# Optimization experiments

Hardware: AMD Instinct MI355X
Metric: run time of the kernel (lower is better)

## Reference

```python
import jax, jax.numpy as jnp
import numpy as np

N = 50000
E = 800000
NFEAT, NHID, NCODE, NCLASS = 512, 256, 64, 40


def setup_inputs() -> dict:
    key = jax.random.key(0)
    ks = jax.random.split(key, 16)
    def glorot(k, shape):
        lim = 1.0 / np.sqrt(shape[0])
        return jax.random.uniform(k, shape, jnp.float32, -lim, lim)
    return {
        "x": jax.random.normal(ks[0], (N, NFEAT), jnp.float32),
        "edge_src": jax.random.randint(ks[1], (E,), 0, N, jnp.int32),
        "edge_dst": jax.random.randint(ks[2], (E,), 0, N, jnp.int32),
        "edge_weight": jax.random.uniform(ks[3], (E,), jnp.float32),
        "eps": jax.random.normal(ks[4], (N, NCODE), jnp.float32),
        # gc1: GraphConvolution(nfeat, nhid)
        "W1": glorot(ks[5], (NFEAT, NHID)),
        "b1": glorot(ks[6], (NHID,)),
        # fc11 / fc12: Linear(nhid, ncode)
        "W_mu": glorot(ks[7], (NHID, NCODE)),
        "b_mu": glorot(ks[8], (NCODE,)),
        "W_lv": glorot(ks[9], (NHID, NCODE)),
        "b_lv": glorot(ks[10], (NCODE,)),
        # fc2: Linear(ncode, nhid)
        "W_dec": glorot(ks[11], (NCODE, NHID)),
        "b_dec": glorot(ks[12], (NHID,)),
        # gc2: GraphConvolution(2*nhid, nclass)
        "W2": glorot(ks[13], (2 * NHID, NCLASS)),
        "b2": glorot(ks[14], (NCLASS,)),
    }


def spmm(edge_src, edge_dst, edge_weight, support):
    # spmm(adj, support): gather rows at src, scale by edge weight, scatter-add to dst
    msgs = support[edge_src] * edge_weight[:, None]  # [E, d]
    return jax.ops.segment_sum(msgs, edge_dst, num_segments=N)


def reference(x, edge_src, edge_dst, edge_weight, eps,
              W1, b1, W_mu, b_mu, W_lv, b_lv, W_dec, b_dec, W2, b2):
    # gc1: relu(spmm(adj, x @ W1) + b1)
    h1 = jax.nn.relu(spmm(edge_src, edge_dst, edge_weight, x @ W1) + b1)
    # dropout is identity in inference mode
    mu = h1 @ W_mu + b_mu
    log_var = h1 @ W_lv + b_lv
    # reparametrize: std = exp(log_var) (as in source, no 0.5 factor)
    z = mu + eps * jnp.exp(log_var)
    # decode
    x1 = jax.nn.relu(z @ W_dec + b_dec)
    x1 = jnp.concatenate([x1, h1], axis=1)  # [N, 2*nhid]
    # gc2
    logits = spmm(edge_src, edge_dst, edge_weight, x1 @ W2) + b2
    return jax.nn.log_softmax(logits, axis=1)
```

## Files before the change

kernel.cpp:

```cpp
#include <hip/hip_runtime.h>
#include <math.h>

#define N_NODES 50000
#define N_EDGES 800000
#define NFEAT 512
#define NHID 256
#define NCODE 64
#define NCLASS 40
#define NCLS_PAD 48
#define NB_SCAN 196

typedef __attribute__((ext_vector_type(8))) short short8;
typedef __attribute__((ext_vector_type(8))) unsigned short ushort8;
typedef __attribute__((ext_vector_type(4))) unsigned short ushort4v;
typedef __attribute__((ext_vector_type(4))) float floatx4;

__device__ inline unsigned short f2bf(float f) {
    unsigned u = __builtin_bit_cast(unsigned, f);
    u += 0x7fff + ((u >> 16) & 1);
    return (unsigned short)(u >> 16);
}
__device__ inline float bf2f(unsigned short h) {
    return __builtin_bit_cast(float, (unsigned)h << 16);
}
__device__ inline unsigned pkbf(float lo, float hi) {
    unsigned r;
    asm("v_cvt_pk_bf16_f32 %0, %1, %2" : "=v"(r) : "v"(lo), "v"(hi));
    return r;
}
__device__ inline void gload_lds16(const void* g, void* l) {
    __builtin_amdgcn_global_load_lds(
        (const __attribute__((address_space(1))) unsigned int*)g,
        (__attribute__((address_space(3))) unsigned int*)l, 16, 0, 0);
}

__global__ __launch_bounds__(256) void hist_kernel(const int* __restrict__ dst,
                                                   int* __restrict__ counts) {
    int t = blockIdx.x * 256 + threadIdx.x;
    if (t < N_EDGES) atomicAdd(&counts[dst[t]], 1);
}

__global__ __launch_bounds__(256) void scan_block_sums(const int* __restrict__ counts,
                                                       int* __restrict__ blockSums) {
    __shared__ int red[256];
    int t = threadIdx.x;
    int i = blockIdx.x * 256 + t;
    red[t] = (i < N_NODES) ? counts[i] : 0;
    __syncthreads();
#pragma unroll
    for (int off = 128; off > 0; off >>= 1) {
        if (t < off) red[t] += red[t + off];
        __syncthreads();
    }
    if (t == 0) blockSums[blockIdx.x] = red[0];
}

__global__ __launch_bounds__(256) void scan_block_offsets(const int* __restrict__ blockSums,
                                                          int* __restrict__ blockOffsets,
                                                          int* __restrict__ offsets) {
    __shared__ int s[256];
    int t = threadIdx.x;
    int v = (t < NB_SCAN) ? blockSums[t] : 0;
    s[t] = v;
    __syncthreads();
#pragma unroll
    for (int off = 1; off < 256; off <<= 1) {
        int x = (t >= off) ? s[t - off] : 0;
        __syncthreads();
        s[t] += x;
        __syncthreads();
    }
    if (t < NB_SCAN) blockOffsets[t] = s[t] - v;
    if (t == 255) offsets[N_NODES] = s[255];
}

__global__ __launch_bounds__(256) void scan_final(const int* __restrict__ counts,
                                                  const int* __restrict__ blockOffsets,
                                                  int* __restrict__ offsets) {
    __shared__ int s[256];
    int t = threadIdx.x;
    int i = blockIdx.x * 256 + t;
    int v = (i < N_NODES) ? counts[i] : 0;
    s[t] = v;
    __syncthreads();
#pragma unroll
    for (int off = 1; off < 256; off <<= 1) {
        int x = (t >= off) ? s[t - off] : 0;
        __syncthreads();
        s[t] += x;
        __syncthreads();
    }
    if (i < N_NODES) offsets[i] = blockOffsets[blockIdx.x] + s[t] - v;
}

__global__ __launch_bounds__(256) void scatter_kernel(const int* __restrict__ dst,
                                                      const int* __restrict__ src,
                                                      const float* __restrict__ w,
                                                      const int* __restrict__ offsets,
                                                      int* __restrict__ cursor,
                                                      int2* __restrict__ edges) {
    int t = blockIdx.x * 256 + threadIdx.x;
    if (t < N_EDGES) {
        int d = dst[t];
        int pos = offsets[d] + atomicAdd(&cursor[d], 1);
        edges[pos] = make_int2(src[t], __builtin_bit_cast(int, w[t]));
    }
}

__global__ __launch_bounds__(256) void wprep_kernel(const float* __restrict__ W1,
                                                    const float* __restrict__ W2,
                                                    const float* __restrict__ W_mu,
                                                    const float* __restrict__ W_lv,
                                                    const float* __restrict__ W_dec,
                                                    unsigned short* __restrict__ W1t,
                                                    unsigned short* __restrict__ W2bt,
                                                    unsigned short* __restrict__ W_mulvt,
                                                    unsigned short* __restrict__ W_dect) {
    int idx = blockIdx.x * 256 + threadIdx.x;
    if (idx < NFEAT * NHID) {
        int k = idx >> 8;
        int n = idx & 255;
        W1t[(size_t)n * NFEAT + k] = f2bf(W1[idx]);
    } else if (idx < NFEAT * NHID + NCLS_PAD * NFEAT) {
        int i2 = idx - NFEAT * NHID;
        int n = i2 >> 9;
        int k = i2 & 511;
        W2bt[i2] = (n < NCLASS) ? f2bf(W2[(size_t)k * NCLASS + n]) : (unsigned short)0;
    } else if (idx < NFEAT * NHID + NCLS_PAD * NFEAT + 128 * 256) {
        int i2 = idx - NFEAT * NHID - NCLS_PAD * NFEAT;
        int j = i2 >> 8;
        int k = i2 & 255;
        float v = (j < 64) ? W_mu[(size_t)k * NCODE + j] : W_lv[(size_t)k * NCODE + (j - 64)];
        W_mulvt[i2] = f2bf(v);
    } else if (idx < NFEAT * NHID + NCLS_PAD * NFEAT + 128 * 256 + 256 * 64) {
        int i2 = idx - NFEAT * NHID - NCLS_PAD * NFEAT - 128 * 256;
        int n = i2 >> 6;
        int k = i2 & 63;
        W_dect[i2] = f2bf(W_dec[(size_t)k * NHID + n]);
    }
}

__global__ __launch_bounds__(256) void gemm1_mfma(const float* __restrict__ A,
                                                  const unsigned short* __restrict__ Bt,
                                                  unsigned short* __restrict__ C) {
    __shared__ unsigned short As[2][128 * 64];
    __shared__ unsigned short Bs[2][128 * 64];
    int t = threadIdx.x;
    int wave = t >> 6, lane = t & 63;
    int quad = lane >> 4, m16 = lane & 15;
    int wr = wave >> 1, wc = wave & 1;
    int m0 = blockIdx.x * 128;
    int n0 = blockIdx.y * 128;

    int srow = t >> 3;
    int kcs = (t & 7) ^ (srow & 7);
    const float* Ap[4];
    const unsigned short* Bp[4];
#pragma unroll
    for (int r = 0; r < 4; ++r) {
        int row = r * 32 + srow;
        int ga = m0 + row;
        if (ga >= N_NODES) ga = N_NODES - 1;
        Ap[r] = A + (size_t)ga * NFEAT + kcs * 8;
        Bp[r] = Bt + (size_t)(n0 + row) * NFEAT + kcs * 8;
    }

    floatx4 acc[4][4];
#pragma unroll
    for (int m = 0; m < 4; ++m)
#pragma unroll
        for (int n = 0; n < 4; ++n) acc[m][n] = (floatx4){0.f, 0.f, 0.f, 0.f};

    float4 a0[4], a1[4];
#pragma unroll
    for (int r = 0; r < 4; ++r)
        gload_lds16(Bp[r], &Bs[0][(r * 256 + wave * 64) * 8]);
#pragma unroll
    for (int r = 0; r < 4; ++r) {
        a0[r] = *(const float4*)(Ap[r]);
        a1[r] = *(const float4*)(Ap[r] + 4);
    }
#pragma unroll
    for (int r = 0; r < 4; ++r) {
        uint4 w;
        w.x = pkbf(a0[r].x, a0[r].y);
        w.y = pkbf(a0[r].z, a0[r].w);
        w.z = pkbf(a1[r].x, a1[r].y);
        w.w = pkbf(a1[r].z, a1[r].w);
        *(uint4*)&As[0][(r * 256 + t) * 8] = w;
    }
    __syncthreads();

#pragma unroll
    for (int k0 = 0; k0 < NFEAT; k0 += 64) {
        const int cur = (k0 >> 6) & 1, nxt = cur ^ 1;
        const bool more = (k0 + 64 < NFEAT);
        if (more) {
#pragma unroll
            for (int r = 0; r < 4; ++r)
                gload_lds16(Bp[r] + (k0 + 64), &Bs[nxt][(r * 256 + wave * 64) * 8]);
#pragma unroll
            for (int r = 0; r < 4; ++r) {
                a0[r] = *(const float4*)(Ap[r] + k0 + 64);
                a1[r] = *(const float4*)(Ap[r] + k0 + 68);
            }
        }
#pragma unroll
        for (int c = 0; c < 2; ++c) {
            int sw = ((c * 4 + quad) ^ (m16 & 7)) * 8;
            short8 af[4], bfr[4];
#pragma unroll
            for (int m = 0; m < 4; ++m)
                af[m] = *(const short8*)&As[cur][(wr * 64 + m * 16 + m16) * 64 + sw];
#pragma unroll
            for (int n = 0; n < 4; ++n)
                bfr[n] = *(const short8*)&Bs[cur][(wc * 64 + n * 16 + m16) * 64 + sw];
#pragma unroll
            for (int m = 0; m < 4; ++m)
#pragma unroll
                for (int n = 0; n < 4; ++n)
                    acc[m][n] =
                        __builtin_amdgcn_mfma_f32_16x16x32_bf16(af[m], bfr[n], acc[m][n], 0, 0, 0);
        }
        if (more) {
#pragma unroll
            for (int r = 0; r < 4; ++r) {
                uint4 w;
                w.x = pkbf(a0[r].x, a0[r].y);
                w.y = pkbf(a0[r].z, a0[r].w);
                w.z = pkbf(a1[r].x, a1[r].y);
                w.w = pkbf(a1[r].z, a1[r].w);
                *(uint4*)&As[nxt][(r * 256 + t) * 8] = w;
            }
            __syncthreads();
        }
    }
#pragma unroll
    for (int m = 0; m < 4; ++m) {
#pragma unroll
        for (int n = 0; n < 4; ++n) {
            int col = n0 + wc * 64 + n * 16 + m16;
#pragma unroll
            for (int r = 0; r < 4; ++r) {
                int row = m0 + wr * 64 + m * 16 + quad * 4 + r;
                if (row < N_NODES) C[(size_t)row * NHID + col] = f2bf(acc[m][n][r]);
            }
        }
    }
}

__global__ __launch_bounds__(256) void spmm1_kernel(const int* __restrict__ offsets,
                                                    const int2* __restrict__ edges,
                                                    const unsigned short* __restrict__ S1b,
                                                    const float* __restrict__ b1,
                                                    unsigned short* __restrict__ x1cat) {
    int n = blockIdx.x * 4 + (threadIdx.x >> 6);
    int lane = threadIdx.x & 63;
    int beg = offsets[n], end = offsets[n + 1];
    float ax = 0.f, ay = 0.f, az = 0.f, aw = 0.f;
    int i = beg;
    for (; i + 8 <= end; i += 8) {
        int2 e[8];
        ushort4v r[8];
#pragma unroll
        for (int u = 0; u < 8; u++) e[u] = edges[i + u];
#pragma unroll
        for (int u = 0; u < 8; u++)
            r[u] = *(const ushort4v*)&S1b[(size_t)e[u].x * NHID + lane * 4];
#pragma unroll
        for (int u = 0; u < 8; u++) {
            float ww = __builtin_bit_cast(float, e[u].y);
            ax += ww * bf2f(r[u][0]);
            ay += ww * bf2f(r[u][1]);
            az += ww * bf2f(r[u][2]);
            aw += ww * bf2f(r[u][3]);
        }
    }
    for (; i < end; i++) {
        int2 e = edges[i];
        float ww = __builtin_bit_cast(float, e.y);
        ushort4v r = *(const ushort4v*)&S1b[(size_t)e.x * NHID + lane * 4];
        ax += ww * bf2f(r[0]); ay += ww * bf2f(r[1]);
        az += ww * bf2f(r[2]); aw += ww * bf2f(r[3]);
    }
    float4 bb = *(const float4*)&b1[lane * 4];
    ushort4v hb;
    hb[0] = f2bf(fmaxf(ax + bb.x, 0.f));
    hb[1] = f2bf(fmaxf(ay + bb.y, 0.f));
    hb[2] = f2bf(fmaxf(az + bb.z, 0.f));
    hb[3] = f2bf(fmaxf(aw + bb.w, 0.f));
    *(ushort4v*)&x1cat[(size_t)n * (2 * NHID) + NHID + lane * 4] = hb;
}

__global__ __launch_bounds__(256) void mlp_mfma(const unsigned short* __restrict__ x1cat_ro,
                                                const float* __restrict__ eps,
                                                const float* __restrict__ b_mu,
                                                const float* __restrict__ b_lv,
                                                const unsigned short* __restrict__ W_mulvt,
                                                const float* __restrict__ b_dec,
                                                const unsigned short* __restrict__ W_dect,
                                                unsigned short* __restrict__ x1cat) {
    __shared__ float smulv[16][132];
    __shared__ unsigned short z_bf[16][72];
    int t = threadIdx.x;
    int wave = t >> 6, lane = t & 63;
    int quad = lane >> 4, m16 = lane & 15;
    int node0 = blockIdx.x * 16;

    {
        floatx4 acc[2];
        acc[0] = (floatx4){0.f, 0.f, 0.f, 0.f};
        acc[1] = (floatx4){0.f, 0.f, 0.f, 0.f};
        const unsigned short* Abase =
            x1cat_ro + (size_t)(node0 + m16) * 512 + 256 + quad * 8;
        const unsigned short* Bb0 = W_mulvt + (size_t)(wave * 32 + m16) * 256 + quad * 8;
        const unsigned short* Bb1 = Bb0 + 16 * 256;
#pragma unroll
        for (int k0 = 0; k0 < 256; k0 += 32) {
            short8 afrag = *(const short8*)(Abase + k0);
            short8 bf0 = *(const short8*)(Bb0 + k0);
            short8 bf1 = *(const short8*)(Bb1 + k0);
            acc[0] = __builtin_amdgcn_mfma_f32_16x16x32_bf16(afrag, bf0, acc[0], 0, 0, 0);
            acc[1] = __builtin_amdgcn_mfma_f32_16x16x32_bf16(afrag, bf1, acc[1], 0, 0, 0);
        }
#pragma unroll
        for (int nt = 0; nt < 2; nt++) {
            int j = wave * 32 + nt * 16 + m16;
            float bias = (j < 64) ? b_mu[j] : b_lv[j - 64];
#pragma unroll
            for (int r = 0; r < 4; r++)
                smulv[quad * 4 + r][j] = acc[nt][r] + bias;
        }
    }
    __syncthreads();
#pragma unroll
    for (int r = 0; r < 4; r++) {
        int idx = t + r * 256;
        int n = idx >> 6, j = idx & 63;
        float z = smulv[n][j] + eps[(size_t)node0 * NCODE + idx] * expf(smulv[n][64 + j]);
        z_bf[n][j] = f2bf(z);
    }
    __syncthreads();
    {
        floatx4 acc[4];
#pragma unroll
        for (int i = 0; i < 4; i++) acc[i] = (floatx4){0.f, 0.f, 0.f, 0.f};
#pragma unroll
        for (int ks = 0; ks < 2; ks++) {
            int k0 = ks * 32;
            short8 afrag = *(const short8*)&z_bf[m16][k0 + quad * 8];
#pragma unroll
            for (int nt = 0; nt < 4; nt++) {
                int col = wave * 64 + nt * 16 + m16;
                short8 bfrag = *(const short8*)(W_dect + (size_t)col * 64 + k0 + quad * 8);
                acc[nt] = __builtin_amdgcn_mfma_f32_16x16x32_bf16(afrag, bfrag, acc[nt], 0, 0, 0);
            }
        }
#pragma unroll
        for (int nt = 0; nt < 4; nt++) {
            int col = wave * 64 + nt * 16 + m16;
            float bias = b_dec[col];
#pragma unroll
            for (int r = 0; r < 4; r++) {
                int node = node0 + quad * 4 + r;
                x1cat[(size_t)node * 512 + col] = f2bf(fmaxf(acc[nt][r] + bias, 0.f));
            }
        }
    }
}

__global__ __launch_bounds__(256) void gemm2_mfma(const unsigned short* __restrict__ Xb,
                                                  const unsigned short* __restrict__ Bt,
                                                  unsigned short* __restrict__ S2b) {
    __shared__ unsigned short Bs[NCLS_PAD][520];
    int t = threadIdx.x;
    int wave = t >> 6, lane = t & 63;
    int quad = lane >> 4, m16 = lane & 15;
    int m0 = blockIdx.x * 64;

#pragma unroll
    for (int r = 0; r < 12; ++r) {
        int cidx = r * 256 + t;
        int row = cidx >> 6, col = (cidx & 63) * 8;
        *(ushort8*)&Bs[row][col] = *(const ushort8*)&Bt[(size_t)row * NFEAT + col];
    }

    int arow = m0 + wave * 16 + m16;
    if (arow >= N_NODES) arow = N_NODES - 1;
    const unsigned short* Abase = Xb + (size_t)arow * NFEAT + quad * 8;

    floatx4 acc[3];
#pragma unroll
    for (int i = 0; i < 3; i++) acc[i] = (floatx4){0.f, 0.f, 0.f, 0.f};
    __syncthreads();

#pragma unroll
    for (int k0 = 0; k0 < NFEAT; k0 += 32) {
        short8 af = *(const short8*)(Abase + k0);
#pragma unroll
        for (int nt = 0; nt < 3; nt++) {
            short8 bfr = *(const short8*)&Bs[nt * 16 + m16][k0 + quad * 8];
            acc[nt] = __builtin_amdgcn_mfma_f32_16x16x32_bf16(af, bfr, acc[nt], 0, 0, 0);
        }
    }
#pragma unroll
    for (int nt = 0; nt < 3; nt++) {
        int col = nt * 16 + m16;
        if (col < NCLASS) {
#pragma unroll
            for (int r = 0; r < 4; r++) {
                int row = m0 + wave * 16 + quad * 4 + r;
                if (row < N_NODES) S2b[(size_t)row * NCLASS + col] = f2bf(acc[nt][r]);
            }
        }
    }
}

__global__ __launch_bounds__(256) void spmm2_softmax_kernel(const int* __restrict__ offsets,
                                                            const int2* __restrict__ edges,
                                                            const unsigned short* __restrict__ S2b,
                                                            const float* __restrict__ b2,
                                                            float* __restrict__ out) {
    int wave = threadIdx.x >> 6;
    int lane = threadIdx.x & 63;
    int n = blockIdx.x * 4 + wave;
    int beg = offsets[n], end = offsets[n + 1];
    float acc = 0.f;
    int i = beg;
    for (; i + 4 <= end; i += 4) {
        int2 e0 = edges[i], e1 = edges[i + 1], e2 = edges[i + 2], e3 = edges[i + 3];
        float w0 = __builtin_bit_cast(float, e0.y);
        float w1 = __builtin_bit_cast(float, e1.y);
        float w2 = __builtin_bit_cast(float, e2.y);
        float w3 = __builtin_bit_cast(float, e3.y);
        if (lane < NCLASS) {
            float v0 = bf2f(S2b[(size_t)e0.x * NCLASS + lane]);
            float v1 = bf2f(S2b[(size_t)e1.x * NCLASS + lane]);
            float v2 = bf2f(S2b[(size_t)e2.x * NCLASS + lane]);
            float v3 = bf2f(S2b[(size_t)e3.x * NCLASS + lane]);
            acc += w0 * v0 + w1 * v1 + w2 * v2 + w3 * v3;
        }
    }
    for (; i < end; i++) {
        int2 e = edges[i];
        float ww = __builtin_bit_cast(float, e.y);
        if (lane < NCLASS) acc += ww * bf2f(S2b[(size_t)e.x * NCLASS + lane]);
    }
    float v = (lane < NCLASS) ? (acc + b2[lane]) : -INFINITY;
    float m = v;
#pragma unroll
    for (int off = 32; off > 0; off >>= 1) m = fmaxf(m, __shfl_xor(m, off));
    float ex = (lane < NCLASS) ? expf(v - m) : 0.f;
    float ssum = ex;
#pragma unroll
    for (int off = 32; off > 0; off >>= 1) ssum += __shfl_xor(ssum, off);
    if (lane < NCLASS) out[(size_t)n * NCLASS + lane] = v - m - logf(ssum);
}

extern "C" void kernel_launch(void* const* d_in, const int* in_sizes, int n_in,
                              void* d_out, int out_size, void* d_ws, size_t ws_size,
                              hipStream_t stream) {
    const float* x     = (const float*)d_in[0];
    const int*   esrc  = (const int*)d_in[1];
    const int*   edst  = (const int*)d_in[2];
    const float* ew    = (const float*)d_in[3];
    const float* eps   = (const float*)d_in[4];
    const float* W1    = (const float*)d_in[5];
    const float* b1    = (const float*)d_in[6];
    const float* W_mu  = (const float*)d_in[7];
    const float* b_mu  = (const float*)d_in[8];
    const float* W_lv  = (const float*)d_in[9];
    const float* b_lv  = (const float*)d_in[10];
    const float* W_dec = (const float*)d_in[11];
    const float* b_dec = (const float*)d_in[12];
    const float* W2    = (const float*)d_in[13];
    const float* b2    = (const float*)d_in[14];
    float* out = (float*)d_out;

    unsigned short* support1b = (unsigned short*)d_ws;
    unsigned short* x1cat = support1b + (size_t)N_NODES * NHID;
    unsigned short* S2b = x1cat + (size_t)N_NODES * 2 * NHID;
    unsigned short* W1t    = S2b + (size_t)N_NODES * NCLASS;
    unsigned short* W2bt   = W1t + (size_t)NHID * NFEAT;
    unsigned short* W_mulvt = W2bt + (size_t)NCLS_PAD * NFEAT;
    unsigned short* W_dect  = W_mulvt + 128 * 256;
    int*   counts   = (int*)(((size_t)(W_dect + 256 * 64) + 3) & ~(size_t)3);
    int*   cursor   = counts + N_NODES;
    int*   offsets  = cursor + N_NODES;
    int*   blockSums    = offsets + N_NODES + 1;
    int*   blockOffsets = blockSums + NB_SCAN;
    int2*  edges    = (int2*)(blockOffsets + NB_SCAN);
    edges = (int2*)(((size_t)edges + 7) & ~(size_t)7);
    size_t need = (size_t)((char*)(edges + N_EDGES) - (char*)d_ws);
    if (ws_size < need) return;

    hipMemsetAsync(counts, 0, 2 * N_NODES * sizeof(int), stream);
    hist_kernel<<<(N_EDGES + 255) / 256, 256, 0, stream>>>(edst, counts);
    scan_block_sums<<<NB_SCAN, 256, 0, stream>>>(counts, blockSums);
    scan_block_offsets<<<1, 256, 0, stream>>>(blockSums, blockOffsets, offsets);
    scan_final<<<NB_SCAN, 256, 0, stream>>>(counts, blockOffsets, offsets);
    scatter_kernel<<<(N_EDGES + 255) / 256, 256, 0, stream>>>(edst, esrc, ew, offsets, cursor,
                                                              edges);

    wprep_kernel<<<800, 256, 0, stream>>>(W1, W2, W_mu, W_lv, W_dec, W1t, W2bt, W_mulvt, W_dect);
    dim3 g1((N_NODES + 127) / 128, 2);
    gemm1_mfma<<<g1, 256, 0, stream>>>(x, W1t, support1b);
    spmm1_kernel<<<N_NODES / 4, 256, 0, stream>>>(offsets, edges, support1b, b1, x1cat);
    mlp_mfma<<<N_NODES / 16, 256, 0, stream>>>(x1cat, eps, b_mu, b_lv, W_mulvt, b_dec, W_dect,
                                               x1cat);
    gemm2_mfma<<<(N_NODES + 63) / 64, 256, 0, stream>>>(x1cat, W2bt, S2b);
    spmm2_softmax_kernel<<<N_NODES / 4, 256, 0, stream>>>(offsets, edges, S2b, b2, out);
}
```

Before: 454.4 us.

## Single-buffer LDS tiles in gemm1 to halve shared memory and raise occupancy

Replaces the double-buffered A and B shared-memory tiles in the first GEMM with single buffers. Each k-step now waits at a barrier, loads the B tile synchronously and stores the converted A tile, then waits at a second barrier. The A register prefetch is kept, but B's global-to-LDS load is no longer overlapped with MFMA compute. The likely aim is to halve LDS per block so more blocks fit per CU, at the cost of an extra barrier and exposed B load latency each iteration.

```diff
diff --git a/kernel.cpp b/kernel.cpp
--- a/kernel.cpp
+++ b/kernel.cpp
@@ -143,8 +143,8 @@
 __global__ __launch_bounds__(256) void gemm1_mfma(const float* __restrict__ A,
                                                   const unsigned short* __restrict__ Bt,
                                                   unsigned short* __restrict__ C) {
-    __shared__ unsigned short As[2][128 * 64];
-    __shared__ unsigned short Bs[2][128 * 64];
+    __shared__ unsigned short As[128 * 64];
+    __shared__ unsigned short Bs[128 * 64];
     int t = threadIdx.x;
     int wave = t >> 6, lane = t & 63;
     int quad = lane >> 4, m16 = lane & 15;
@@ -155,15 +155,13 @@
     int srow = t >> 3;
     int kcs = (t & 7) ^ (srow & 7);
     const float* Ap[4];
-    const unsigned short* Bp[4];
 #pragma unroll
     for (int r = 0; r < 4; ++r) {
-        int row = r * 32 + srow;
-        int ga = m0 + row;
+        int ga = m0 + r * 32 + srow;
         if (ga >= N_NODES) ga = N_NODES - 1;
         Ap[r] = A + (size_t)ga * NFEAT + kcs * 8;
-        Bp[r] = Bt + (size_t)(n0 + row) * NFEAT + kcs * 8;
-    }
+    }
+    const unsigned short* Bbase = Bt + (size_t)(n0 + srow) * NFEAT + kcs * 8;
 
     floatx4 acc[4][4];
 #pragma unroll
@@ -172,33 +170,30 @@
         for (int n = 0; n < 4; ++n) acc[m][n] = (floatx4){0.f, 0.f, 0.f, 0.f};
 
     float4 a0[4], a1[4];
-#pragma unroll
-    for (int r = 0; r < 4; ++r)
-        gload_lds16(Bp[r], &Bs[0][(r * 256 + wave * 64) * 8]);
 #pragma unroll
     for (int r = 0; r < 4; ++r) {
         a0[r] = *(const float4*)(Ap[r]);
         a1[r] = *(const float4*)(Ap[r] + 4);
     }
-#pragma unroll
-    for (int r = 0; r < 4; ++r) {
-        uint4 w;
-        w.x = pkbf(a0[r].x, a0[r].y);
-        w.y = pkbf(a0[r].z, a0[r].w);
-        w.z = pkbf(a1[r].x, a1[r].y);
-        w.w = pkbf(a1[r].z, a1[r].w);
-        *(uint4*)&As[0][(r * 256 + t) * 8] = w;
-    }
-    __syncthreads();
 
 #pragma unroll
     for (int k0 = 0; k0 < NFEAT; k0 += 64) {
-        const int cur = (k0 >> 6) & 1, nxt = cur ^ 1;
-        const bool more = (k0 + 64 < NFEAT);
-        if (more) {
-#pragma unroll
-            for (int r = 0; r < 4; ++r)
-                gload_lds16(Bp[r] + (k0 + 64), &Bs[nxt][(r * 256 + wave * 64) * 8]);
+        uint4 aw[4];
+#pragma unroll
+        for (int r = 0; r < 4; ++r) {
+            aw[r].x = pkbf(a0[r].x, a0[r].y);
+            aw[r].y = pkbf(a0[r].z, a0[r].w);
+            aw[r].z = pkbf(a1[r].x, a1[r].y);
+            aw[r].w = pkbf(a1[r].z, a1[r].w);
+        }
+        __syncthreads();
+#pragma unroll
+        for (int r = 0; r < 4; ++r)
+            gload_lds16(Bbase + (size_t)r * 32 * NFEAT + k0, &Bs[(r * 256 + wave * 64) * 8]);
+#pragma unroll
+        for (int r = 0; r < 4; ++r) *(uint4*)&As[(r * 256 + t) * 8] = aw[r];
+        __syncthreads();
+        if (k0 + 64 < NFEAT) {
 #pragma unroll
             for (int r = 0; r < 4; ++r) {
                 a0[r] = *(const float4*)(Ap[r] + k0 + 64);
@@ -211,28 +206,16 @@
             short8 af[4], bfr[4];
 #pragma unroll
             for (int m = 0; m < 4; ++m)
-                af[m] = *(const short8*)&As[cur][(wr * 64 + m * 16 + m16) * 64 + sw];
+                af[m] = *(const short8*)&As[(wr * 64 + m * 16 + m16) * 64 + sw];
 #pragma unroll
             for (int n = 0; n < 4; ++n)
-                bfr[n] = *(const short8*)&Bs[cur][(wc * 64 + n * 16 + m16) * 64 + sw];
+                bfr[n] = *(const short8*)&Bs[(wc * 64 + n * 16 + m16) * 64 + sw];
 #pragma unroll
             for (int m = 0; m < 4; ++m)
 #pragma unroll
                 for (int n = 0; n < 4; ++n)
                     acc[m][n] =
                         __builtin_amdgcn_mfma_f32_16x16x32_bf16(af[m], bfr[n], acc[m][n], 0, 0, 0);
-        }
-        if (more) {
-#pragma unroll
-            for (int r = 0; r < 4; ++r) {
-                uint4 w;
-                w.x = pkbf(a0[r].x, a0[r].y);
-                w.y = pkbf(a0[r].z, a0[r].w);
-                w.z = pkbf(a1[r].x, a1[r].y);
-                w.w = pkbf(a1[r].z, a1[r].w);
-                *(uint4*)&As[nxt][(r * 256 + t) * 8] = w;
-            }
-            __syncthreads();
         }
     }
 #pragma unroll
```

Measured after the change: 452.2 us. No clear change (-0.5%).
